# Optimization experiments

Measured on AMD Instinct MI355X. Metric: run time of the kernel, lower is better.

The kernel has to match this reference:

```python
import jax, jax.numpy as jnp
from jax import lax
import numpy as np
import math

B, N, A = 4096, 8, 5
IN_CH, HW = 3, 5
POS = 2
OBS_IN = POS + N            # 10
OBS_ACT_IN = OBS_IN + A     # 15
D = 128                     # obs_output_dim == d_k == embed width
STATE_DIM = 32 + OBS_IN     # 42
SAP_IN = 32 + OBS_ACT_IN    # 47


def setup_inputs() -> dict:
    key = jax.random.key(0)
    ks = jax.random.split(key, 24)
    w = lambda k, shape: (jax.random.normal(k, shape) * 0.05).astype(jnp.float32)
    return {
        "agent_states": jax.random.normal(ks[0], (B, N, IN_CH, HW, HW), jnp.float32),
        "agent_global_positions": jax.random.normal(ks[1], (B, N, POS), jnp.float32),
        "agent_one_hot_encoding": jax.random.uniform(ks[2], (B, N, N), jnp.float32),
        "policies": jax.random.uniform(ks[3], (B, N, A), jnp.float32),
        "actions": jax.random.uniform(ks[4], (B, N, A), jnp.float32),
        "conv1_w": w(ks[5], (16, IN_CH, 3, 3)), "conv1_b": w(ks[6], (16,)),
        "conv2_w": w(ks[7], (32, 16, 3, 3)),    "conv2_b": w(ks[8], (32,)),
        "se_w": w(ks[9], (STATE_DIM, 128)),     "se_b": w(ks[10], (128,)),
        "key_w": w(ks[11], (128, D)),           "key_b": w(ks[12], (D,)),
        "query_w": w(ks[13], (128, D)),         "query_b": w(ks[14], (D,)),
        "sap_w": w(ks[15], (SAP_IN, 128)),      "sap_b": w(ks[16], (128,)),
        "av_w": w(ks[17], (128, 128)),          "av_b": w(ks[18], (128,)),
        "f1_w": w(ks[19], (128, 64)),           "f1_b": w(ks[20], (64,)),
        "f2_w": w(ks[21], (64, 1)),             "f2_b": w(ks[22], (1,)),
    }


def _conv(x, w, b):
    y = lax.conv_general_dilated(x, w, (1, 1), 'VALID',
                                 dimension_numbers=('NCHW', 'OIHW', 'NCHW'))
    return y + b[None, :, None, None]


def reference(agent_states, agent_global_positions, agent_one_hot_encoding,
              policies, actions,
              conv1_w, conv1_b, conv2_w, conv2_b,
              se_w, se_b, key_w, key_b, query_w, query_b,
              sap_w, sap_b, av_w, av_b, f1_w, f1_b, f2_w, f2_b):
    leaky = lambda x: jnp.where(x >= 0, x, 0.01 * x)
    b, n = agent_states.shape[0], agent_states.shape[1]

    # CNN encoder: [B*N,3,5,5] -> [B*N,32,1,1]
    x = agent_states.reshape(b * n, IN_CH, HW, HW)
    h = leaky(_conv(x, conv1_w, conv1_b))
    h = leaky(_conv(h, conv2_w, conv2_b))
    pose_id = jnp.concatenate([agent_global_positions, agent_one_hot_encoding], axis=-1)
    states = jnp.concatenate([h.reshape(b, n, -1), pose_id], axis=-1)  # [B,N,42]

    states_embed = jnp.tanh(states @ se_w + se_b)                      # [B,N,128]
    k = states_embed @ key_w + key_b
    q = states_embed @ query_w + query_b
    weight = jax.nn.softmax(jnp.einsum('bqd,bkd->bqk', q, k) / math.sqrt(D), axis=-1)

    obs_actions = jnp.concatenate([states, actions], axis=-1)          # [B,N,47]
    obs_policy = jnp.concatenate([states, policies], axis=-1)         # [B,N,47]
    # place_policies puts the policy vector on the diagonal (i==j), action elsewhere.
    eye = jnp.eye(n, dtype=states.dtype)[None, :, :, None]             # [1,N,N,1]
    oap = eye * obs_policy[:, None, :, :] + (1.0 - eye) * obs_actions[:, None, :, :]  # [B,i,j,47]

    oap_embed = jnp.tanh(oap @ sap_w + sap_b)                          # [B,N,N,128]
    attn_vals = jnp.tanh(oap_embed @ av_w + av_b)                      # [B,i,j,128]

    # node_features[b,a,i,d] = sum_j weight[b,a,j] * attn_vals[b,i,j,d]
    # (replaces the original repeat -> broadcast-multiply -> sum over O(N^4) tensor)
    node_features = jnp.einsum('baj,bijd->baid', weight, attn_vals)    # [B,N,N,128]

    v = jnp.tanh(node_features @ f1_w + f1_b)
    value = v @ f2_w + f2_b                                            # [B,N,N,1]
    return value, weight
```

## Files before the change

### kernel.cpp

```cpp
#include <hip/hip_runtime.h>
#include <math.h>

#define NB 4096
#define NA 8
#define BN (NB*NA)

#define OFF_SE   0
#define OFF_SAP  4096
#define OFF_AV   8192
#define OFF_F1   16384
#define OFF_M    20480
#define OFF_U    28672
#define OFF_W2P  28800

typedef short short8 __attribute__((ext_vector_type(8)));
typedef float f32x4 __attribute__((ext_vector_type(4)));

#define MFMA(a,b,c) __builtin_amdgcn_mfma_f32_16x16x32_bf16(a,b,c,0,0,0)

__device__ __forceinline__ float fast_tanh(float x){
    float e = __expf(2.0f*x);
    return 1.0f - 2.0f*__builtin_amdgcn_rcpf(e+1.0f);
}
__device__ __forceinline__ unsigned bfr(float x){
    unsigned u = __float_as_uint(x);
    return (u + 0x7fffu + ((u>>16)&1u)) >> 16;
}
__device__ __forceinline__ unsigned pk2(float lo, float hi){
    return bfr(lo) | (bfr(hi)<<16);
}
__device__ __forceinline__ float bf2f(unsigned short s){
    return __uint_as_float(((unsigned)s)<<16);
}
__device__ __forceinline__ short8 fragld(const unsigned* p){
    union { uint4 u; short8 s; } cv;
    cv.u = *(const uint4*)p;
    return cv.s;
}

__global__ __launch_bounds__(256) void kW(const float* __restrict__ se_w,
        const float* __restrict__ sap_w, const float* __restrict__ av_w,
        const float* __restrict__ f1_w, const float* __restrict__ qw,
        const float* __restrict__ kw, const float* __restrict__ qb,
        const float* __restrict__ w2,
        unsigned* __restrict__ ws){
    int idx = blockIdx.x*256 + threadIdx.x;
    if (idx < 4096){
        int w = idx, tile = w>>9, rem = w&511;
        int ft = rem>>6, r2 = (rem>>2)&15, wi = rem&3;
        int f2 = tile*16 + r2, f1 = ft*8 + wi*2;
        float lo = (f1   < 42)? se_w[f1*128+f2]     : 0.f;
        float hi = (f1+1 < 42)? se_w[(f1+1)*128+f2] : 0.f;
        ws[OFF_SE + w] = pk2(lo,hi);
    } else if (idx < 8192){
        int w = idx-4096, tile = w>>9, rem = w&511;
        int ft = rem>>6, r2 = (rem>>2)&15, wi = rem&3;
        int f2 = tile*16 + r2, f1 = ft*8 + wi*2;
        float lo = (f1   < 47)? sap_w[f1*128+f2]     : 0.f;
        float hi = (f1+1 < 47)? sap_w[(f1+1)*128+f2] : 0.f;
        ws[OFF_SAP + w] = pk2(lo,hi);
    } else if (idx < 16384){
        int w = idx-8192, tile = w>>10, rem = w&1023;
        int ft = rem>>6, r2 = (rem>>2)&15, wi = rem&3;
        int f2 = tile*16 + r2, f1 = ft*8 + wi*2;
        ws[OFF_AV + w] = pk2(av_w[f1*128+f2], av_w[(f1+1)*128+f2]);
    } else if (idx < 20480){
        int w = idx-16384, tile = w>>10, rem = w&1023;
        int ft = rem>>6, r2 = (rem>>2)&15, wi = rem&3;
        int f2 = tile*16 + r2, f1 = ft*8 + wi*2;
        ws[OFF_F1 + w] = pk2(f1_w[f1*64+f2], f1_w[(f1+1)*64+f2]);
    } else if (idx < 28672){
        int w = idx-20480, tile = w>>10, rem = w&1023;
        int ft = rem>>6, r2 = (rem>>2)&15, wi = rem&3;
        int f2 = tile*16 + r2, e0 = ft*8 + wi*2;
        float lo=0.f, hi=0.f;
        for (int d=0; d<128; ++d){
            float kv = kw[f2*128+d];
            lo += qw[e0*128+d]*kv;
            hi += qw[(e0+1)*128+d]*kv;
        }
        ws[OFF_M + w] = pk2(lo,hi);
    } else if (idx < 28800){
        int f = idx-28672;
        float a = 0.f;
        for (int d=0; d<128; ++d) a += qb[d]*kw[f*128+d];
        ((float*)ws)[OFF_U + f] = a;
    } else if (idx < 31360){
        int w = idx-28800;
        int ftile = w/1280, rem = w - ftile*1280;
        int ft = rem>>6, r2 = (rem>>2)&15, wi = rem&3;
        int f = ftile*16 + r2, k0 = ft*8 + wi*2;
        float lo = (k0   < 144)? w2[f*144+k0]   : 0.f;
        float hi = (k0+1 < 144)? w2[f*144+k0+1] : 0.f;
        ws[OFF_W2P + w] = pk2(lo,hi);
    }
}

__global__ __launch_bounds__(256,2) void kF(const unsigned* __restrict__ ws,
        const float* __restrict__ xin, const float* __restrict__ pos,
        const float* __restrict__ oneh, const float* __restrict__ acts,
        const float* __restrict__ pols,
        const float* __restrict__ w1, const float* __restrict__ b1,
        const float* __restrict__ b2,
        const float* __restrict__ se_b,
        const float* __restrict__ sap_b, const float* __restrict__ av_b,
        const float* __restrict__ f1_b, const float* __restrict__ f2_w,
        const float* __restrict__ f2_b,
        float* __restrict__ wout, float* __restrict__ value){
    __shared__ unsigned SM[9216];
    __shared__ unsigned stPk[4096];
    __shared__ unsigned sA64[2176];
    __shared__ unsigned sP64[2176];
    __shared__ float s_w[512];
    __shared__ float s_bias[384];
    __shared__ float s_ub[256];
    const int t = threadIdx.x;
    const int wv = t>>6, lane = t&63;
    const int g = lane>>4, c = lane&15;

    float* c_in   = (float*)SM;
    unsigned* hpk = SM + 1216;
    float* c_ap   = (float*)(SM+6336);
    float* c_pose = (float*)(SM+6496);
    float* c_w1   = (float*)(SM+6656);
    float* c_b1   = (float*)(SM+7088);
    float* c_b2   = (float*)(SM+7104);
    for (int q=t; q<432; q+=256) c_w1[q] = w1[q];
    if (t<16) c_b1[t] = b1[t];
    if (t<32) c_b2[t] = b2[t];
    for (int q=t; q<512; q+=256) hpk[(q>>7)*1280 + 1152 + (q&127)] = 0;
    for (int q=t; q<384; q+=256)
        s_bias[q] = (q<128)? sap_b[q] : (q<256)? av_b[q-128] : (q<320)? f1_b[q-256] : f2_w[q-320];
    s_ub[t] = (t<128)? ((const float*)ws)[OFF_U+t] : se_b[t-128];

    for (int p=0; p<4; ++p){
        const size_t a0g = (size_t)blockIdx.x*64 + p*16;
        for (int q=t; q<1200; q+=256){
            int ag=q/75, r=q-ag*75;
            c_in[ag*76+r] = xin[a0g*75+q];
        }
        for (int q=t; q<160; q+=256){
            int ag=q/10, k=q-ag*10;
            c_ap[q]   = (k<5)? acts[(a0g+ag)*5+k] : pols[(a0g+ag)*5+(k-5)];
            c_pose[q] = (k<2)? pos[(a0g+ag)*2+k]  : oneh[(a0g+ag)*8+(k-2)];
        }
        __syncthreads();
        {
            const int ag = t&15, oc = t>>4;
            float w[27];
            #pragma unroll
            for (int i=0;i<27;++i) w[i]=c_w1[oc*27+i];
            float out[9];
            float bb = c_b1[oc];
            #pragma unroll
            for (int q=0;q<9;++q) out[q]=bb;
            #pragma unroll
            for (int ic=0;ic<3;++ic){
                float pin[25];
                #pragma unroll
                for (int i=0;i<25;++i) pin[i]=c_in[ag*76+ic*25+i];
                #pragma unroll
                for (int y=0;y<3;++y)
                  #pragma unroll
                  for (int x=0;x<3;++x)
                    #pragma unroll
                    for (int ky=0;ky<3;++ky)
                      #pragma unroll
                      for (int kx=0;kx<3;++kx)
                        out[y*3+x] += pin[(y+ky)*5+(x+kx)] * w[ic*9+ky*3+kx];
            }
            unsigned short* hp16 = (unsigned short*)(hpk + p*1280);
            #pragma unroll
            for (int q=0;q<9;++q){
                float v = out[q];
                v = (v>=0.f)? v : 0.01f*v;
                int k = oc*9+q;
                int word = (k>>3)*64 + ag*4 + ((k>>1)&3);
                hp16[word*2 + (k&1)] = (unsigned short)bfr(v);
            }
        }
        {
            const int ft4 = t>>6, r = (t>>2)&15, wi = t&3;
            const int f0 = 32 + ft4*8 + wi*2;
            float a0=0.f,a1=0.f,p0=0.f,p1=0.f;
            if (f0 < 42){ a0 = c_pose[r*10 + f0-32]; p0 = a0; }
            else if (f0 < 47){ a0 = c_ap[r*10 + f0-42]; p0 = c_ap[r*10+5 + f0-42]; }
            if (f0+1 < 42){ a1 = c_pose[r*10 + f0-31]; p1 = a1; }
            else if (f0+1 < 47){ a1 = c_ap[r*10 + f0-41]; p1 = c_ap[r*10+5 + f0-41]; }
            int word = p*512 + (4+ft4)*64 + r*4 + wi;
            stPk[word]      = pk2(a0,a1);
            stPk[2048+word] = pk2(p0,p1);
        }
        __syncthreads();
    }
    {
        const unsigned* hw = hpk + wv*1280;
        f32x4 c2[2];
        c2[0] = (f32x4){0.f,0.f,0.f,0.f};
        c2[1] = (f32x4){0.f,0.f,0.f,0.f};
        #pragma unroll
        for (int kt=0; kt<5; ++kt){
            short8 hb  = fragld(hw + kt*256 + lane*4);
            short8 w0f = fragld(ws + OFF_W2P + kt*256 + lane*4);
            short8 w1f = fragld(ws + OFF_W2P + 1280 + kt*256 + lane*4);
            c2[0] = MFMA(w0f, hb, c2[0]);
            c2[1] = MFMA(w1f, hb, c2[1]);
        }
        #pragma unroll
        for (int ft=0; ft<2; ++ft){
            const float* bp = &c_b2[ft*16 + g*4];
            float d0 = c2[ft][0]+bp[0]; d0 = (d0>=0.f)? d0 : 0.01f*d0;
            float d1 = c2[ft][1]+bp[1]; d1 = (d1>=0.f)? d1 : 0.01f*d1;
            float d2 = c2[ft][2]+bp[2]; d2 = (d2>=0.f)? d2 : 0.01f*d2;
            float d3 = c2[ft][3]+bp[3]; d3 = (d3>=0.f)? d3 : 0.01f*d3;
            int word = wv*512 + (2*ft + (g>>1))*64 + c*4 + (g&1)*2;
            uint2 pw = make_uint2(pk2(d0,d1), pk2(d2,d3));
            *(uint2*)&stPk[word] = pw;
            *(uint2*)&stPk[2048+word] = pw;
        }
    }
    __syncthreads();

    const int tile = blockIdx.x*4 + wv;
    short8 bfA0 = fragld(&stPk[wv*512 + lane*4]);
    short8 bfA1 = fragld(&stPk[wv*512 + 256 + lane*4]);
    short8 bfP0 = fragld(&stPk[2048 + wv*512 + lane*4]);
    short8 bfP1 = fragld(&stPk[2048 + wv*512 + 256 + lane*4]);
    unsigned (*s_stage)[2048] = (unsigned (*)[2048])&SM[0];
    unsigned* U1 = &SM[4096];
    unsigned* wS = &U1[wv*1280];
    unsigned* tS = &U1[wv*1280 + 1024];

    uint4 r0, r1;
#define PREF(off) { r0 = *(const uint4*)(ws + (off) + t*4); \
                    r1 = *(const uint4*)(ws + (off) + 1024 + t*4); }
#define WR(b) { *(uint4*)&s_stage[b][t*4] = r0; *(uint4*)&s_stage[b][1024 + t*4] = r1; }

    PREF(OFF_SE); WR(0);
    __syncthreads();

    f32x4 acc[8];
    #pragma unroll
    for (int i=0;i<8;++i) acc[i] = (f32x4){0.f,0.f,0.f,0.f};
    PREF(OFF_SE + 2048);
    #pragma unroll
    for (int ft=0; ft<4; ++ft){
        short8 a0 = fragld(&s_stage[0][ft*512 + lane*4]);
        short8 a1 = fragld(&s_stage[0][ft*512 + 256 + lane*4]);
        acc[ft] = MFMA(a0, bfA0, acc[ft]);
        acc[ft] = MFMA(a1, bfA1, acc[ft]);
    }
    WR(1); __syncthreads();
    PREF(OFF_M);
    #pragma unroll
    for (int ft=4; ft<8; ++ft){
        short8 a0 = fragld(&s_stage[1][(ft-4)*512 + lane*4]);
        short8 a1 = fragld(&s_stage[1][(ft-4)*512 + 256 + lane*4]);
        acc[ft] = MFMA(a0, bfA0, acc[ft]);
        acc[ft] = MFMA(a1, bfA1, acc[ft]);
    }
    WR(0);
    #pragma unroll
    for (int ft=0; ft<8; ++ft){
        const float* bp = &s_ub[128 + ft*16 + g*4];
        float d0 = fast_tanh(acc[ft][0]+bp[0]);
        float d1 = fast_tanh(acc[ft][1]+bp[1]);
        float d2 = fast_tanh(acc[ft][2]+bp[2]);
        float d3 = fast_tanh(acc[ft][3]+bp[3]);
        int word = (2*ft + (g>>1))*64 + c*4 + (g&1)*2;
        *(uint2*)&wS[word] = make_uint2(pk2(d0,d1), pk2(d2,d3));
    }
    short8 ef[4];
    #pragma unroll
    for (int kt=0; kt<4; ++kt) ef[kt] = fragld(&wS[kt*256 + lane*4]);
    __syncthreads();

    f32x4 L = (f32x4){0.f,0.f,0.f,0.f};
    #pragma unroll
    for (int i=0; i<4; ++i){
        const int nextOff = (i<3)? (OFF_M + (i+1)*2048) : OFF_SAP;
        PREF(nextOff);
        f32x4 a2[2];
        a2[0] = (f32x4){0.f,0.f,0.f,0.f};
        a2[1] = (f32x4){0.f,0.f,0.f,0.f};
        #pragma unroll
        for (int ftl=0; ftl<2; ++ftl)
          #pragma unroll
          for (int kt=0; kt<4; ++kt){
            short8 mf = fragld(&s_stage[i&1][ftl*1024 + kt*256 + lane*4]);
            a2[ftl] = MFMA(mf, ef[kt], a2[ftl]);
          }
        WR((i+1)&1);
        #pragma unroll
        for (int ftl=0; ftl<2; ++ftl){
            const float* up = &s_ub[(2*i+ftl)*16 + g*4];
            int word = (2*ftl + (g>>1))*64 + c*4 + (g&1)*2;
            *(uint2*)&tS[word] = make_uint2(pk2(a2[ftl][0]+up[0], a2[ftl][1]+up[1]),
                                            pk2(a2[ftl][2]+up[2], a2[ftl][3]+up[3]));
        }
        short8 tf = fragld(&tS[lane*4]);
        L = MFMA(tf, ef[i], L);
        __syncthreads();
    }
    {
        float sc[4];
        #pragma unroll
        for (int q=0;q<4;++q) sc[q] = L[q]*0.08838834764831845f;
        #pragma unroll
        for (int q=0;q<4;++q){
            float m = sc[q];
            m = fmaxf(m, __shfl_xor(m,1));
            m = fmaxf(m, __shfl_xor(m,2));
            m = fmaxf(m, __shfl_xor(m,4));
            float ex = __expf(sc[q]-m);
            float su = ex;
            su += __shfl_xor(su,1);
            su += __shfl_xor(su,2);
            su += __shfl_xor(su,4);
            sc[q] = ex/su;
        }
        if ((c>>3) == (g>>1)){
            int lb = wv*2 + (g>>1);
            int batch = tile*2 + (g>>1);
            int idx = ((g&1)*4)*8 + (c&7);
            #pragma unroll
            for (int q=0;q<4;++q){
                float v = sc[q];
                wout[batch*64 + idx + q*8] = v;
                s_w[lb*64 + idx + q*8] = v;
            }
        }
    }

    f32x4 aS[2][8];
    #pragma unroll
    for (int v=0;v<2;++v)
      #pragma unroll
      for (int i=0;i<8;++i) aS[v][i] = (f32x4){0.f,0.f,0.f,0.f};
    PREF(OFF_SAP + 2048);
    #pragma unroll
    for (int ft=0; ft<4; ++ft){
        short8 a0 = fragld(&s_stage[0][ft*512 + lane*4]);
        short8 a1 = fragld(&s_stage[0][ft*512 + 256 + lane*4]);
        aS[0][ft] = MFMA(a0, bfA0, aS[0][ft]);
        aS[0][ft] = MFMA(a1, bfA1, aS[0][ft]);
        aS[1][ft] = MFMA(a0, bfP0, aS[1][ft]);
        aS[1][ft] = MFMA(a1, bfP1, aS[1][ft]);
    }
    WR(1); __syncthreads();
    PREF(OFF_AV);
    #pragma unroll
    for (int ft=4; ft<8; ++ft){
        short8 a0 = fragld(&s_stage[1][(ft-4)*512 + lane*4]);
        short8 a1 = fragld(&s_stage[1][(ft-4)*512 + 256 + lane*4]);
        aS[0][ft] = MFMA(a0, bfA0, aS[0][ft]);
        aS[0][ft] = MFMA(a1, bfA1, aS[0][ft]);
        aS[1][ft] = MFMA(a0, bfP0, aS[1][ft]);
        aS[1][ft] = MFMA(a1, bfP1, aS[1][ft]);
    }
    WR(0);
    short8 spA[4], spP[4];
    #pragma unroll
    for (int ft=0; ft<8; ++ft){
        const float* bp = &s_bias[ft*16 + g*4];
        float d0 = fast_tanh(aS[0][ft][0]+bp[0]);
        float d1 = fast_tanh(aS[0][ft][1]+bp[1]);
        float d2 = fast_tanh(aS[0][ft][2]+bp[2]);
        float d3 = fast_tanh(aS[0][ft][3]+bp[3]);
        int word = (2*ft + (g>>1))*64 + c*4 + (g&1)*2;
        *(uint2*)&wS[word] = make_uint2(pk2(d0,d1), pk2(d2,d3));
    }
    #pragma unroll
    for (int kt=0; kt<4; ++kt) spA[kt] = fragld(&wS[kt*256 + lane*4]);
    #pragma unroll
    for (int ft=0; ft<8; ++ft){
        const float* bp = &s_bias[ft*16 + g*4];
        float d0 = fast_tanh(aS[1][ft][0]+bp[0]);
        float d1 = fast_tanh(aS[1][ft][1]+bp[1]);
        float d2 = fast_tanh(aS[1][ft][2]+bp[2]);
        float d3 = fast_tanh(aS[1][ft][3]+bp[3]);
        int word = (2*ft + (g>>1))*64 + c*4 + (g&1)*2;
        *(uint2*)&wS[word] = make_uint2(pk2(d0,d1), pk2(d2,d3));
    }
    #pragma unroll
    for (int kt=0; kt<4; ++kt) spP[kt] = fragld(&wS[kt*256 + lane*4]);
    __syncthreads();

    f32x4 aV[2][8];
    #pragma unroll
    for (int v=0;v<2;++v)
      #pragma unroll
      for (int i=0;i<8;++i) aV[v][i] = (f32x4){0.f,0.f,0.f,0.f};
    short8 avA[4], avP[4];
    #pragma unroll
    for (int i=0; i<4; ++i){
        const int nextOff = (i<3)? (OFF_AV + (i+1)*2048) : OFF_F1;
        PREF(nextOff);
        #pragma unroll
        for (int ftl=0; ftl<2; ++ftl){
            const int ft = 2*i + ftl;
            #pragma unroll
            for (int kt=0; kt<4; ++kt){
                short8 af = fragld(&s_stage[i&1][ftl*1024 + kt*256 + lane*4]);
                aV[0][ft] = MFMA(af, spA[kt], aV[0][ft]);
                aV[1][ft] = MFMA(af, spP[kt], aV[1][ft]);
            }
        }
        WR((i+1)&1);
        if (i==3){
            #pragma unroll
            for (int ft=0; ft<8; ++ft){
                const float* bp = &s_bias[128 + ft*16 + g*4];
                float d0 = fast_tanh(aV[0][ft][0]+bp[0]);
                float d1 = fast_tanh(aV[0][ft][1]+bp[1]);
                float d2 = fast_tanh(aV[0][ft][2]+bp[2]);
                float d3 = fast_tanh(aV[0][ft][3]+bp[3]);
                int word = (2*ft + (g>>1))*64 + c*4 + (g&1)*2;
                *(uint2*)&wS[word] = make_uint2(pk2(d0,d1), pk2(d2,d3));
            }
            #pragma unroll
            for (int kt=0; kt<4; ++kt) avA[kt] = fragld(&wS[kt*256 + lane*4]);
            #pragma unroll
            for (int ft=0; ft<8; ++ft){
                const float* bp = &s_bias[128 + ft*16 + g*4];
                float d0 = fast_tanh(aV[1][ft][0]+bp[0]);
                float d1 = fast_tanh(aV[1][ft][1]+bp[1]);
                float d2 = fast_tanh(aV[1][ft][2]+bp[2]);
                float d3 = fast_tanh(aV[1][ft][3]+bp[3]);
                int word = (2*ft + (g>>1))*64 + c*4 + (g&1)*2;
                *(uint2*)&wS[word] = make_uint2(pk2(d0,d1), pk2(d2,d3));
            }
            #pragma unroll
            for (int kt=0; kt<4; ++kt) avP[kt] = fragld(&wS[kt*256 + lane*4]);
        }
        __syncthreads();
    }

    f32x4 aF[2][4];
    #pragma unroll
    for (int v=0;v<2;++v)
      #pragma unroll
      for (int i=0;i<4;++i) aF[v][i] = (f32x4){0.f,0.f,0.f,0.f};
    PREF(OFF_F1 + 2048);
    #pragma unroll
    for (int ftl=0; ftl<2; ++ftl)
      #pragma unroll
      for (int kt=0; kt<4; ++kt){
        short8 af = fragld(&s_stage[0][ftl*1024 + kt*256 + lane*4]);
        aF[0][ftl] = MFMA(af, avA[kt], aF[0][ftl]);
        aF[1][ftl] = MFMA(af, avP[kt], aF[1][ftl]);
      }
    WR(1); __syncthreads();
    #pragma unroll
    for (int ftl=0; ftl<2; ++ftl)
      #pragma unroll
      for (int kt=0; kt<4; ++kt){
        short8 af = fragld(&s_stage[1][ftl*1024 + kt*256 + lane*4]);
        aF[0][2+ftl] = MFMA(af, avA[kt], aF[0][2+ftl]);
        aF[1][2+ftl] = MFMA(af, avP[kt], aF[1][2+ftl]);
      }
    {
        int row = wv*16 + c;
        #pragma unroll
        for (int v=0;v<2;++v){
            unsigned* dst = v? sP64 : sA64;
            #pragma unroll
            for (int ft=0; ft<4; ++ft){
                int idx = row*34 + ft*8 + 2*g;
                *(uint2*)&dst[idx] = make_uint2(pk2(aF[v][ft][0], aF[v][ft][1]),
                                                pk2(aF[v][ft][2], aF[v][ft][3]));
            }
        }
    }
    __syncthreads();
    float* s_b64 = (float*)U1;
    const unsigned short* A16 = (const unsigned short*)sA64;
    const unsigned short* P16 = (const unsigned short*)sP64;
    #pragma unroll
    for (int k=0; k<16; ++k){
        int e = t + 256*k;
        int bq = e>>9, a = (e>>6)&7, cc = e&63;
        const float* wp = &s_w[bq*64 + a*8];
        float acc4 = 0.f;
        #pragma unroll
        for (int j=0;j<8;++j) acc4 += wp[j]*bf2f(A16[(bq*8+j)*68 + cc]);
        s_b64[(bq*8+a)*68 + cc] = acc4;
    }
    __syncthreads();
    #pragma unroll
    for (int k=0; k<2; ++k){
        int o = t + 256*k;
        int bq = o>>6, a = (o>>3)&7, i = o&7;
        float w_ai = s_w[bq*64 + a*8 + i];
        const float* pb = &s_b64[(bq*8+a)*68];
        const unsigned short* pA = &A16[(bq*8+i)*68];
        const unsigned short* pP = &P16[(bq*8+i)*68];
        float acc5 = 0.f;
        #pragma unroll 8
        for (int cc=0; cc<64; ++cc){
            float dd = bf2f(pP[cc]) - bf2f(pA[cc]);
            acc5 += fast_tanh(pb[cc] + w_ai*dd + s_bias[256+cc]) * s_bias[320+cc];
        }
        value[(size_t)blockIdx.x*512 + o] = acc5 + f2_b[0];
    }
#undef PREF
#undef WR
}

extern "C" void kernel_launch(void* const* d_in, const int* in_sizes, int n_in,
                              void* d_out, int out_size, void* d_ws, size_t ws_size,
                              hipStream_t stream){
    const float* agent_states = (const float*)d_in[0];
    const float* pos    = (const float*)d_in[1];
    const float* oneh   = (const float*)d_in[2];
    const float* pols   = (const float*)d_in[3];
    const float* acts   = (const float*)d_in[4];
    const float* w1     = (const float*)d_in[5];
    const float* b1     = (const float*)d_in[6];
    const float* w2     = (const float*)d_in[7];
    const float* b2     = (const float*)d_in[8];
    const float* se_w   = (const float*)d_in[9];
    const float* se_b   = (const float*)d_in[10];
    const float* key_w  = (const float*)d_in[11];
    const float* query_w= (const float*)d_in[13];
    const float* query_b= (const float*)d_in[14];
    const float* sap_w  = (const float*)d_in[15];
    const float* sap_b  = (const float*)d_in[16];
    const float* av_w   = (const float*)d_in[17];
    const float* av_b   = (const float*)d_in[18];
    const float* f1_w   = (const float*)d_in[19];
    const float* f1_b   = (const float*)d_in[20];
    const float* f2_w   = (const float*)d_in[21];
    const float* f2_b   = (const float*)d_in[22];

    unsigned* ws = (unsigned*)d_ws;

    float* value = (float*)d_out;
    float* wout  = value + (size_t)NB*NA*NA;

    kW<<<123, 256, 0, stream>>>(se_w, sap_w, av_w, f1_w, query_w, key_w, query_b, w2, ws);
    kF<<<BN/64, 256, 0, stream>>>(ws, agent_states, pos, oneh, acts, pols,
                                  w1, b1, b2, se_b, sap_b, av_b, f1_b, f2_w, f2_b,
                                  wout, value);
}
```

Baseline: 52.44 us.

## Double block size to 512 threads, splitting each tile's feature work across two waves

```diff
diff --git a/kernel.cpp b/kernel.cpp
--- a/kernel.cpp
+++ b/kernel.cpp
@@ -96,7 +96,7 @@
     }
 }
 
-__global__ __launch_bounds__(256,2) void kF(const unsigned* __restrict__ ws,
+__global__ __launch_bounds__(512,4) void kF(const unsigned* __restrict__ ws,
         const float* __restrict__ xin, const float* __restrict__ pos,
         const float* __restrict__ oneh, const float* __restrict__ acts,
         const float* __restrict__ pols,
@@ -117,36 +117,38 @@
     const int t = threadIdx.x;
     const int wv = t>>6, lane = t&63;
     const int g = lane>>4, c = lane&15;
+    const int tl = wv>>1, h = wv&1;
 
     float* c_in   = (float*)SM;
-    unsigned* hpk = SM + 1216;
-    float* c_ap   = (float*)(SM+6336);
-    float* c_pose = (float*)(SM+6496);
-    float* c_w1   = (float*)(SM+6656);
-    float* c_b1   = (float*)(SM+7088);
-    float* c_b2   = (float*)(SM+7104);
-    for (int q=t; q<432; q+=256) c_w1[q] = w1[q];
-    if (t<16) c_b1[t] = b1[t];
-    if (t<32) c_b2[t] = b2[t];
-    for (int q=t; q<512; q+=256) hpk[(q>>7)*1280 + 1152 + (q&127)] = 0;
-    for (int q=t; q<384; q+=256)
-        s_bias[q] = (q<128)? sap_b[q] : (q<256)? av_b[q-128] : (q<320)? f1_b[q-256] : f2_w[q-320];
-    s_ub[t] = (t<128)? ((const float*)ws)[OFF_U+t] : se_b[t-128];
-
-    for (int p=0; p<4; ++p){
-        const size_t a0g = (size_t)blockIdx.x*64 + p*16;
-        for (int q=t; q<1200; q+=256){
-            int ag=q/75, r=q-ag*75;
-            c_in[ag*76+r] = xin[a0g*75+q];
-        }
-        for (int q=t; q<160; q+=256){
-            int ag=q/10, k=q-ag*10;
-            c_ap[q]   = (k<5)? acts[(a0g+ag)*5+k] : pols[(a0g+ag)*5+(k-5)];
-            c_pose[q] = (k<2)? pos[(a0g+ag)*2+k]  : oneh[(a0g+ag)*8+(k-2)];
+    unsigned* hpk = SM + 2432;
+    float* c_ap   = (float*)(SM+7552);
+    float* c_pose = (float*)(SM+7872);
+    float* c_w1   = (float*)(SM+8192);
+    float* c_b1   = (float*)(SM+8624);
+    float* c_b2   = (float*)(SM+8640);
+    if (t<432) c_w1[t] = w1[t];
+    else if (t<448) c_b1[t-432] = b1[t-432];
+    else if (t<480) c_b2[t-448] = b2[t-448];
+    hpk[(t>>7)*1280 + 1152 + (t&127)] = 0;
+    if (t<384)
+        s_bias[t] = (t<128)? sap_b[t] : (t<256)? av_b[t-128] : (t<320)? f1_b[t-256] : f2_w[t-320];
+    if (t<256) s_ub[t] = (t<128)? ((const float*)ws)[OFF_U+t] : se_b[t-128];
+
+    for (int p=0; p<2; ++p){
+        for (int q=t; q<2400; q+=512){
+            int tp=q/1200, rr=q-tp*1200, ag=rr/75, r=rr-ag*75;
+            size_t row = (size_t)blockIdx.x*64 + (p*2+tp)*16 + ag;
+            c_in[tp*1216 + ag*76 + r] = xin[row*75 + r];
+        }
+        if (t<320){
+            int tp=t/160, rr=t-tp*160, ag=rr/10, k=rr-ag*10;
+            size_t row = (size_t)blockIdx.x*64 + (p*2+tp)*16 + ag;
+            c_ap[t]   = (k<5)? acts[row*5+k] : pols[row*5+(k-5)];
+            c_pose[t] = (k<2)? pos[row*2+k]  : oneh[row*8+(k-2)];
         }
         __syncthreads();
         {
-            const int ag = t&15, oc = t>>4;
+            const int tp = t>>8, tt = t&255, ag = tt&15, oc = tt>>4;
             float w[27];
             #pragma unroll
             for (int i=0;i<27;++i) w[i]=c_w1[oc*27+i];
@@ -158,7 +160,7 @@
             for (int ic=0;ic<3;++ic){
                 float pin[25];
                 #pragma unroll
-                for (int i=0;i<25;++i) pin[i]=c_in[ag*76+ic*25+i];
+                for (int i=0;i<25;++i) pin[i]=c_in[tp*1216 + ag*76 + ic*25 + i];
                 #pragma unroll
                 for (int y=0;y<3;++y)
                   #pragma unroll
@@ -169,7 +171,7 @@
                       for (int kx=0;kx<3;++kx)
                         out[y*3+x] += pin[(y+ky)*5+(x+kx)] * w[ic*9+ky*3+kx];
             }
-            unsigned short* hp16 = (unsigned short*)(hpk + p*1280);
+            unsigned short* hp16 = (unsigned short*)(hpk + (p*2+tp)*1280);
             #pragma unroll
             for (int q=0;q<9;++q){
                 float v = out[q];
@@ -180,20 +182,21 @@
             }
         }
         {
-            const int ft4 = t>>6, r = (t>>2)&15, wi = t&3;
+            const int tp = t>>8, tt = t&255;
+            const int ft4 = tt>>6, r = (tt>>2)&15, wi = tt&3;
             const int f0 = 32 + ft4*8 + wi*2;
             float a0=0.f,a1=0.f,p0=0.f,p1=0.f;
-            if (f0 < 42){ a0 = c_pose[r*10 + f0-32]; p0 = a0; }
-            else if (f0 < 47){ a0 = c_ap[r*10 + f0-42]; p0 = c_ap[r*10+5 + f0-42]; }
-            if (f0+1 < 42){ a1 = c_pose[r*10 + f0-31]; p1 = a1; }
-            else if (f0+1 < 47){ a1 = c_ap[r*10 + f0-41]; p1 = c_ap[r*10+5 + f0-41]; }
-            int word = p*512 + (4+ft4)*64 + r*4 + wi;
+            if (f0 < 42){ a0 = c_pose[tp*160 + r*10 + f0-32]; p0 = a0; }
+            else if (f0 < 47){ a0 = c_ap[tp*160 + r*10 + f0-42]; p0 = c_ap[tp*160 + r*10+5 + f0-42]; }
+            if (f0+1 < 42){ a1 = c_pose[tp*160 + r*10 + f0-31]; p1 = a1; }
+            else if (f0+1 < 47){ a1 = c_ap[tp*160 + r*10 + f0-41]; p1 = c_ap[tp*160 + r*10+5 + f0-41]; }
+            int word = (p*2+tp)*512 + (4+ft4)*64 + r*4 + wi;
             stPk[word]      = pk2(a0,a1);
             stPk[2048+word] = pk2(p0,p1);
         }
         __syncthreads();
     }
-    {
+    if (wv < 4){
         const unsigned* hw = hpk + wv*1280;
         f32x4 c2[2];
         c2[0] = (f32x4){0.f,0.f,0.f,0.f};
@@ -221,88 +224,91 @@
     }
     __syncthreads();
 
-    const int tile = blockIdx.x*4 + wv;
-    short8 bfA0 = fragld(&stPk[wv*512 + lane*4]);
-    short8 bfA1 = fragld(&stPk[wv*512 + 256 + lane*4]);
-    short8 bfP0 = fragld(&stPk[2048 + wv*512 + lane*4]);
-    short8 bfP1 = fragld(&stPk[2048 + wv*512 + 256 + lane*4]);
-    unsigned (*s_stage)[2048] = (unsigned (*)[2048])&SM[0];
-    unsigned* U1 = &SM[4096];
-    unsigned* wS = &U1[wv*1280];
-    unsigned* tS = &U1[wv*1280 + 1024];
+    const int tile = blockIdx.x*4 + tl;
+    short8 bfA0 = fragld(&stPk[tl*512 + lane*4]);
+    short8 bfA1 = fragld(&stPk[tl*512 + 256 + lane*4]);
+    short8 bfP0 = fragld(&stPk[2048 + tl*512 + lane*4]);
+    short8 bfP1 = fragld(&stPk[2048 + tl*512 + 256 + lane*4]);
+    unsigned* stage = SM;
+    unsigned* U1 = SM + 4096;
+    unsigned* wS = U1 + tl*1280;
 
     uint4 r0, r1;
-#define PREF(off) { r0 = *(const uint4*)(ws + (off) + t*4); \
-                    r1 = *(const uint4*)(ws + (off) + 1024 + t*4); }
-#define WR(b) { *(uint4*)&s_stage[b][t*4] = r0; *(uint4*)&s_stage[b][1024 + t*4] = r1; }
-
-    PREF(OFF_SE); WR(0);
-    __syncthreads();
-
-    f32x4 acc[8];
-    #pragma unroll
-    for (int i=0;i<8;++i) acc[i] = (f32x4){0.f,0.f,0.f,0.f};
-    PREF(OFF_SE + 2048);
-    #pragma unroll
-    for (int ft=0; ft<4; ++ft){
-        short8 a0 = fragld(&s_stage[0][ft*512 + lane*4]);
-        short8 a1 = fragld(&s_stage[0][ft*512 + 256 + lane*4]);
-        acc[ft] = MFMA(a0, bfA0, acc[ft]);
-        acc[ft] = MFMA(a1, bfA1, acc[ft]);
-    }
-    WR(1); __syncthreads();
-    PREF(OFF_M);
-    #pragma unroll
-    for (int ft=4; ft<8; ++ft){
-        short8 a0 = fragld(&s_stage[1][(ft-4)*512 + lane*4]);
-        short8 a1 = fragld(&s_stage[1][(ft-4)*512 + 256 + lane*4]);
-        acc[ft] = MFMA(a0, bfA0, acc[ft]);
-        acc[ft] = MFMA(a1, bfA1, acc[ft]);
-    }
-    WR(0);
-    #pragma unroll
-    for (int ft=0; ft<8; ++ft){
+#define PREFP(off) { r0 = *(const uint4*)(ws + (off) + t*4); \
+                     r1 = *(const uint4*)(ws + (off) + 2048 + t*4); }
+#define WRP() { *(uint4*)&stage[t*4] = r0; *(uint4*)&stage[2048 + t*4] = r1; }
+
+    PREFP(OFF_SE);
+    WRP();
+    PREFP(OFF_M);
+    __syncthreads();
+
+    f32x4 acc[4];
+    #pragma unroll
+    for (int i=0;i<4;++i) acc[i] = (f32x4){0.f,0.f,0.f,0.f};
+    #pragma unroll
+    for (int i=0;i<4;++i){
+        short8 a0 = fragld(&stage[h*2048 + i*512 + lane*4]);
+        short8 a1 = fragld(&stage[h*2048 + i*512 + 256 + lane*4]);
+        acc[i] = MFMA(a0, bfA0, acc[i]);
+        acc[i] = MFMA(a1, bfA1, acc[i]);
+    }
+    #pragma unroll
+    for (int i=0;i<4;++i){
+        int ft = h*4+i;
         const float* bp = &s_ub[128 + ft*16 + g*4];
-        float d0 = fast_tanh(acc[ft][0]+bp[0]);
-        float d1 = fast_tanh(acc[ft][1]+bp[1]);
-        float d2 = fast_tanh(acc[ft][2]+bp[2]);
-        float d3 = fast_tanh(acc[ft][3]+bp[3]);
+        float d0 = fast_tanh(acc[i][0]+bp[0]);
+        float d1 = fast_tanh(acc[i][1]+bp[1]);
+        float d2 = fast_tanh(acc[i][2]+bp[2]);
+        float d3 = fast_tanh(acc[i][3]+bp[3]);
         int word = (2*ft + (g>>1))*64 + c*4 + (g&1)*2;
         *(uint2*)&wS[word] = make_uint2(pk2(d0,d1), pk2(d2,d3));
     }
+    __syncthreads();
     short8 ef[4];
     #pragma unroll
     for (int kt=0; kt<4; ++kt) ef[kt] = fragld(&wS[kt*256 + lane*4]);
     __syncthreads();
-
-    f32x4 L = (f32x4){0.f,0.f,0.f,0.f};
-    #pragma unroll
-    for (int i=0; i<4; ++i){
-        const int nextOff = (i<3)? (OFF_M + (i+1)*2048) : OFF_SAP;
-        PREF(nextOff);
-        f32x4 a2[2];
-        a2[0] = (f32x4){0.f,0.f,0.f,0.f};
-        a2[1] = (f32x4){0.f,0.f,0.f,0.f};
-        #pragma unroll
-        for (int ftl=0; ftl<2; ++ftl)
-          #pragma unroll
-          for (int kt=0; kt<4; ++kt){
-            short8 mf = fragld(&s_stage[i&1][ftl*1024 + kt*256 + lane*4]);
-            a2[ftl] = MFMA(mf, ef[kt], a2[ftl]);
-          }
-        WR((i+1)&1);
-        #pragma unroll
-        for (int ftl=0; ftl<2; ++ftl){
-            const float* up = &s_ub[(2*i+ftl)*16 + g*4];
-            int word = (2*ftl + (g>>1))*64 + c*4 + (g&1)*2;
-            *(uint2*)&tS[word] = make_uint2(pk2(a2[ftl][0]+up[0], a2[ftl][1]+up[1]),
-                                            pk2(a2[ftl][2]+up[2], a2[ftl][3]+up[3]));
-        }
-        short8 tf = fragld(&tS[lane*4]);
-        L = MFMA(tf, ef[i], L);
-        __syncthreads();
-    }
+    WRP();
+    PREFP(OFF_M + 4096);
+    __syncthreads();
+    if (h==0){
+        #pragma unroll
+        for (int fl=0; fl<4; ++fl){
+            f32x4 a2 = (f32x4){0.f,0.f,0.f,0.f};
+            #pragma unroll
+            for (int kt=0; kt<4; ++kt)
+                a2 = MFMA(fragld(&stage[fl*1024 + kt*256 + lane*4]), ef[kt], a2);
+            const float* up = &s_ub[fl*16 + g*4];
+            int word = (2*fl + (g>>1))*64 + c*4 + (g&1)*2;
+            *(uint2*)&wS[word] = make_uint2(pk2(a2[0]+up[0], a2[1]+up[1]),
+                                            pk2(a2[2]+up[2], a2[3]+up[3]));
+        }
+    }
+    __syncthreads();
+    WRP();
+    PREFP(OFF_SAP);
+    __syncthreads();
+    if (h==1){
+        #pragma unroll
+        for (int fl=0; fl<4; ++fl){
+            int ft = 4+fl;
+            f32x4 a2 = (f32x4){0.f,0.f,0.f,0.f};
+            #pragma unroll
+            for (int kt=0; kt<4; ++kt)
+                a2 = MFMA(fragld(&stage[fl*1024 + kt*256 + lane*4]), ef[kt], a2);
+            const float* up = &s_ub[ft*16 + g*4];
+            int word = (2*ft + (g>>1))*64 + c*4 + (g&1)*2;
+            *(uint2*)&wS[word] = make_uint2(pk2(a2[0]+up[0], a2[1]+up[1]),
+                                            pk2(a2[2]+up[2], a2[3]+up[3]));
+        }
+    }
+    __syncthreads();
     {
+        f32x4 L = (f32x4){0.f,0.f,0.f,0.f};
+        #pragma unroll
+        for (int kt=0; kt<4; ++kt)
+            L = MFMA(fragld(&wS[kt*256 + lane*4]), ef[kt], L);
         float sc[4];
         #pragma unroll
         for (int q=0;q<4;++q) sc[q] = L[q]*0.08838834764831845f;
@@ -319,8 +325,8 @@
             su += __shfl_xor(su,4);
             sc[q] = ex/su;
         }
-        if ((c>>3) == (g>>1)){
-            int lb = wv*2 + (g>>1);
+        if (h==0 && (c>>3) == (g>>1)){
+            int lb = tl*2 + (g>>1);
             int batch = tile*2 + (g>>1);
             int idx = ((g&1)*4)*8 + (c&7);
             #pragma unroll
@@ -331,144 +337,146 @@
             }
         }
     }
-
-    f32x4 aS[2][8];
+    __syncthreads();
+    WRP();
+    PREFP(OFF_AV);
+    __syncthreads();
+    f32x4 aS[2][4];
     #pragma unroll
     for (int v=0;v<2;++v)
       #pragma unroll
-      for (int i=0;i<8;++i) aS[v][i] = (f32x4){0.f,0.f,0.f,0.f};
-    PREF(OFF_SAP + 2048);
-    #pragma unroll
-    for (int ft=0; ft<4; ++ft){
-        short8 a0 = fragld(&s_stage[0][ft*512 + lane*4]);
-        short8 a1 = fragld(&s_stage[0][ft*512 + 256 + lane*4]);
-        aS[0][ft] = MFMA(a0, bfA0, aS[0][ft]);
-        aS[0][ft] = MFMA(a1, bfA1, aS[0][ft]);
-        aS[1][ft] = MFMA(a0, bfP0, aS[1][ft]);
-        aS[1][ft] = MFMA(a1, bfP1, aS[1][ft]);
-    }
-    WR(1); __syncthreads();
-    PREF(OFF_AV);
-    #pragma unroll
-    for (int ft=4; ft<8; ++ft){
-        short8 a0 = fragld(&s_stage[1][(ft-4)*512 + lane*4]);
-        short8 a1 = fragld(&s_stage[1][(ft-4)*512 + 256 + lane*4]);
-        aS[0][ft] = MFMA(a0, bfA0, aS[0][ft]);
-        aS[0][ft] = MFMA(a1, bfA1, aS[0][ft]);
-        aS[1][ft] = MFMA(a0, bfP0, aS[1][ft]);
-        aS[1][ft] = MFMA(a1, bfP1, aS[1][ft]);
-    }
-    WR(0);
+      for (int i=0;i<4;++i) aS[v][i] = (f32x4){0.f,0.f,0.f,0.f};
+    #pragma unroll
+    for (int i=0;i<4;++i){
+        short8 a0 = fragld(&stage[h*2048 + i*512 + lane*4]);
+        short8 a1 = fragld(&stage[h*2048 + i*512 + 256 + lane*4]);
+        aS[0][i] = MFMA(a0, bfA0, aS[0][i]);
+        aS[0][i] = MFMA(a1, bfA1, aS[0][i]);
+        aS[1][i] = MFMA(a0, bfP0, aS[1][i]);
+        aS[1][i] = MFMA(a1, bfP1, aS[1][i]);
+    }
     short8 spA[4], spP[4];
     #pragma unroll
-    for (int ft=0; ft<8; ++ft){
+    for (int i=0;i<4;++i){
+        int ft = h*4+i;
         const float* bp = &s_bias[ft*16 + g*4];
-        float d0 = fast_tanh(aS[0][ft][0]+bp[0]);
-        float d1 = fast_tanh(aS[0][ft][1]+bp[1]);
-        float d2 = fast_tanh(aS[0][ft][2]+bp[2]);
-        float d3 = fast_tanh(aS[0][ft][3]+bp[3]);
+        float d0 = fast_tanh(aS[0][i][0]+bp[0]);
+        float d1 = fast_tanh(aS[0][i][1]+bp[1]);
+        float d2 = fast_tanh(aS[0][i][2]+bp[2]);
+        float d3 = fast_tanh(aS[0][i][3]+bp[3]);
         int word = (2*ft + (g>>1))*64 + c*4 + (g&1)*2;
         *(uint2*)&wS[word] = make_uint2(pk2(d0,d1), pk2(d2,d3));
     }
+    __syncthreads();
     #pragma unroll
     for (int kt=0; kt<4; ++kt) spA[kt] = fragld(&wS[kt*256 + lane*4]);
-    #pragma unroll
-    for (int ft=0; ft<8; ++ft){
+    __syncthreads();
+    #pragma unroll
+    for (int i=0;i<4;++i){
+        int ft = h*4+i;
         const float* bp = &s_bias[ft*16 + g*4];
-        float d0 = fast_tanh(aS[1][ft][0]+bp[0]);
-        float d1 = fast_tanh(aS[1][ft][1]+bp[1]);
-        float d2 = fast_tanh(aS[1][ft][2]+bp[2]);
-        float d3 = fast_tanh(aS[1][ft][3]+bp[3]);
+        float d0 = fast_tanh(aS[1][i][0]+bp[0]);
+        float d1 = fast_tanh(aS[1][i][1]+bp[1]);
+        float d2 = fast_tanh(aS[1][i][2]+bp[2]);
+        float d3 = fast_tanh(aS[1][i][3]+bp[3]);
         int word = (2*ft + (g>>1))*64 + c*4 + (g&1)*2;
         *(uint2*)&wS[word] = make_uint2(pk2(d0,d1), pk2(d2,d3));
     }
+    __syncthreads();
     #pragma unroll
     for (int kt=0; kt<4; ++kt) spP[kt] = fragld(&wS[kt*256 + lane*4]);
     __syncthreads();
-
-    f32x4 aV[2][8];
+    WRP();
+    PREFP(OFF_AV + 4096);
+    __syncthreads();
+    f32x4 aV[2][4];
     #pragma unroll
     for (int v=0;v<2;++v)
       #pragma unroll
-      for (int i=0;i<8;++i) aV[v][i] = (f32x4){0.f,0.f,0.f,0.f};
+      for (int i=0;i<4;++i) aV[v][i] = (f32x4){0.f,0.f,0.f,0.f};
+    #pragma unroll
+    for (int j=0;j<2;++j){
+        int fl = 2*h + j;
+        #pragma unroll
+        for (int kt=0; kt<4; ++kt){
+            short8 af = fragld(&stage[fl*1024 + kt*256 + lane*4]);
+            aV[0][j] = MFMA(af, spA[kt], aV[0][j]);
+            aV[1][j] = MFMA(af, spP[kt], aV[1][j]);
+        }
+    }
+    __syncthreads();
+    WRP();
+    PREFP(OFF_F1);
+    __syncthreads();
+    #pragma unroll
+    for (int j=0;j<2;++j){
+        int fl = 2*h + j;
+        #pragma unroll
+        for (int kt=0; kt<4; ++kt){
+            short8 af = fragld(&stage[fl*1024 + kt*256 + lane*4]);
+            aV[0][2+j] = MFMA(af, spA[kt], aV[0][2+j]);
+            aV[1][2+j] = MFMA(af, spP[kt], aV[1][2+j]);
+        }
+    }
     short8 avA[4], avP[4];
     #pragma unroll
-    for (int i=0; i<4; ++i){
-        const int nextOff = (i<3)? (OFF_AV + (i+1)*2048) : OFF_F1;
-        PREF(nextOff);
-        #pragma unroll
-        for (int ftl=0; ftl<2; ++ftl){
-            const int ft = 2*i + ftl;
-            #pragma unroll
-            for (int kt=0; kt<4; ++kt){
-                short8 af = fragld(&s_stage[i&1][ftl*1024 + kt*256 + lane*4]);
-                aV[0][ft] = MFMA(af, spA[kt], aV[0][ft]);
-                aV[1][ft] = MFMA(af, spP[kt], aV[1][ft]);
-            }
-        }
-        WR((i+1)&1);
-        if (i==3){
-            #pragma unroll
-            for (int ft=0; ft<8; ++ft){
-                const float* bp = &s_bias[128 + ft*16 + g*4];
-                float d0 = fast_tanh(aV[0][ft][0]+bp[0]);
-                float d1 = fast_tanh(aV[0][ft][1]+bp[1]);
-                float d2 = fast_tanh(aV[0][ft][2]+bp[2]);
-                float d3 = fast_tanh(aV[0][ft][3]+bp[3]);
-                int word = (2*ft + (g>>1))*64 + c*4 + (g&1)*2;
-                *(uint2*)&wS[word] = make_uint2(pk2(d0,d1), pk2(d2,d3));
-            }
-            #pragma unroll
-            for (int kt=0; kt<4; ++kt) avA[kt] = fragld(&wS[kt*256 + lane*4]);
-            #pragma unroll
-            for (int ft=0; ft<8; ++ft){
-                const float* bp = &s_bias[128 + ft*16 + g*4];
-                float d0 = fast_tanh(aV[1][ft][0]+bp[0]);
-                float d1 = fast_tanh(aV[1][ft][1]+bp[1]);
-                float d2 = fast_tanh(aV[1][ft][2]+bp[2]);
-                float d3 = fast_tanh(aV[1][ft][3]+bp[3]);
-                int word = (2*ft + (g>>1))*64 + c*4 + (g&1)*2;
-                *(uint2*)&wS[word] = make_uint2(pk2(d0,d1), pk2(d2,d3));
-            }
-            #pragma unroll
-            for (int kt=0; kt<4; ++kt) avP[kt] = fragld(&wS[kt*256 + lane*4]);
-        }
-        __syncthreads();
-    }
-
-    f32x4 aF[2][4];
+    for (int k=0;k<4;++k){
+        int ft = (k>>1)*4 + 2*h + (k&1);
+        const float* bp = &s_bias[128 + ft*16 + g*4];
+        float d0 = fast_tanh(aV[0][k][0]+bp[0]);
+        float d1 = fast_tanh(aV[0][k][1]+bp[1]);
+        float d2 = fast_tanh(aV[0][k][2]+bp[2]);
+        float d3 = fast_tanh(aV[0][k][3]+bp[3]);
+        int word = (2*ft + (g>>1))*64 + c*4 + (g&1)*2;
+        *(uint2*)&wS[word] = make_uint2(pk2(d0,d1), pk2(d2,d3));
+    }
+    __syncthreads();
+    #pragma unroll
+    for (int kt=0; kt<4; ++kt) avA[kt] = fragld(&wS[kt*256 + lane*4]);
+    __syncthreads();
+    #pragma unroll
+    for (int k=0;k<4;++k){
+        int ft = (k>>1)*4 + 2*h + (k&1);
+        const float* bp = &s_bias[128 + ft*16 + g*4];
+        float d0 = fast_tanh(aV[1][k][0]+bp[0]);
+        float d1 = fast_tanh(aV[1][k][1]+bp[1]);
+        float d2 = fast_tanh(aV[1][k][2]+bp[2]);
+        float d3 = fast_tanh(aV[1][k][3]+bp[3]);
+        int word = (2*ft + (g>>1))*64 + c*4 + (g&1)*2;
+        *(uint2*)&wS[word] = make_uint2(pk2(d0,d1), pk2(d2,d3));
+    }
+    __syncthreads();
+    #pragma unroll
+    for (int kt=0; kt<4; ++kt) avP[kt] = fragld(&wS[kt*256 + lane*4]);
+    __syncthreads();
+    WRP();
+    __syncthreads();
+    f32x4 aF[2][2];
     #pragma unroll
     for (int v=0;v<2;++v)
       #pragma unroll
-      for (int i=0;i<4;++i) aF[v][i] = (f32x4){0.f,0.f,0.f,0.f};
-    PREF(OFF_F1 + 2048);
-    #pragma unroll
-    for (int ftl=0; ftl<2; ++ftl)
-      #pragma unroll
-      for (int kt=0; kt<4; ++kt){
-        short8 af = fragld(&s_stage[0][ftl*1024 + kt*256 + lane*4]);
-        aF[0][ftl] = MFMA(af, avA[kt], aF[0][ftl]);
-        aF[1][ftl] = MFMA(af, avP[kt], aF[1][ftl]);
-      }
-    WR(1); __syncthreads();
-    #pragma unroll
-    for (int ftl=0; ftl<2; ++ftl)
-      #pragma unroll
-      for (int kt=0; kt<4; ++kt){
-        short8 af = fragld(&s_stage[1][ftl*1024 + kt*256 + lane*4]);
-        aF[0][2+ftl] = MFMA(af, avA[kt], aF[0][2+ftl]);
-        aF[1][2+ftl] = MFMA(af, avP[kt], aF[1][2+ftl]);
-      }
+      for (int j=0;j<2;++j) aF[v][j] = (f32x4){0.f,0.f,0.f,0.f};
+    #pragma unroll
+    for (int j=0;j<2;++j){
+        int fl = 2*h + j;
+        #pragma unroll
+        for (int kt=0; kt<4; ++kt){
+            short8 af = fragld(&stage[fl*1024 + kt*256 + lane*4]);
+            aF[0][j] = MFMA(af, avA[kt], aF[0][j]);
+            aF[1][j] = MFMA(af, avP[kt], aF[1][j]);
+        }
+    }
     {
-        int row = wv*16 + c;
+        int row = tl*16 + c;
         #pragma unroll
         for (int v=0;v<2;++v){
             unsigned* dst = v? sP64 : sA64;
             #pragma unroll
-            for (int ft=0; ft<4; ++ft){
+            for (int j=0;j<2;++j){
+                int ft = 2*h + j;
                 int idx = row*34 + ft*8 + 2*g;
-                *(uint2*)&dst[idx] = make_uint2(pk2(aF[v][ft][0], aF[v][ft][1]),
-                                                pk2(aF[v][ft][2], aF[v][ft][3]));
+                *(uint2*)&dst[idx] = make_uint2(pk2(aF[v][j][0], aF[v][j][1]),
+                                                pk2(aF[v][j][2], aF[v][j][3]));
             }
         }
     }
@@ -477,8 +485,8 @@
     const unsigned short* A16 = (const unsigned short*)sA64;
     const unsigned short* P16 = (const unsigned short*)sP64;
     #pragma unroll
-    for (int k=0; k<16; ++k){
-        int e = t + 256*k;
+    for (int k=0; k<8; ++k){
+        int e = t + 512*k;
         int bq = e>>9, a = (e>>6)&7, cc = e&63;
         const float* wp = &s_w[bq*64 + a*8];
         float acc4 = 0.f;
@@ -487,10 +495,8 @@
         s_b64[(bq*8+a)*68 + cc] = acc4;
     }
     __syncthreads();
-    #pragma unroll
-    for (int k=0; k<2; ++k){
-        int o = t + 256*k;
-        int bq = o>>6, a = (o>>3)&7, i = o&7;
+    {
+        int bq = t>>6, a = (t>>3)&7, i = t&7;
         float w_ai = s_w[bq*64 + a*8 + i];
         const float* pb = &s_b64[(bq*8+a)*68];
         const unsigned short* pA = &A16[(bq*8+i)*68];
@@ -501,10 +507,10 @@
             float dd = bf2f(pP[cc]) - bf2f(pA[cc]);
             acc5 += fast_tanh(pb[cc] + w_ai*dd + s_bias[256+cc]) * s_bias[320+cc];
         }
-        value[(size_t)blockIdx.x*512 + o] = acc5 + f2_b[0];
-    }
-#undef PREF
-#undef WR
+        value[(size_t)blockIdx.x*512 + t] = acc5 + f2_b[0];
+    }
+#undef PREFP
+#undef WRP
 }
 
 extern "C" void kernel_launch(void* const* d_in, const int* in_sizes, int n_in,
@@ -539,7 +545,7 @@
     float* wout  = value + (size_t)NB*NA*NA;
 
     kW<<<123, 256, 0, stream>>>(se_w, sap_w, av_w, f1_w, query_w, key_w, query_b, w2, ws);
-    kF<<<BN/64, 256, 0, stream>>>(ws, agent_states, pos, oneh, acts, pols,
+    kF<<<BN/64, 512, 0, stream>>>(ws, agent_states, pos, oneh, acts, pols,
                                   w1, b1, b2, se_b, sap_b, av_b, f1_b, f2_w, f2_b,
                                   wout, value);
 }
```

Measured after the change: 60.00 us. +14.4%, slower.

## Halve fused kernel block to two waves and shrink shared memory footprint

Applied to the files above, without the earlier changes.

```diff
diff --git a/kernel.cpp b/kernel.cpp
--- a/kernel.cpp
+++ b/kernel.cpp
@@ -96,7 +96,7 @@
     }
 }
 
-__global__ __launch_bounds__(256,2) void kF(const unsigned* __restrict__ ws,
+__global__ __launch_bounds__(128,2) void kF(const unsigned* __restrict__ ws,
         const float* __restrict__ xin, const float* __restrict__ pos,
         const float* __restrict__ oneh, const float* __restrict__ acts,
         const float* __restrict__ pols,
@@ -107,46 +107,49 @@
         const float* __restrict__ f1_b, const float* __restrict__ f2_w,
         const float* __restrict__ f2_b,
         float* __restrict__ wout, float* __restrict__ value){
-    __shared__ unsigned SM[9216];
-    __shared__ unsigned stPk[4096];
-    __shared__ unsigned sA64[2176];
-    __shared__ unsigned sP64[2176];
-    __shared__ float s_w[512];
+    __shared__ unsigned SM[6144];
+    __shared__ unsigned stPkA[1024];
+    __shared__ unsigned stP5[128];
+    __shared__ unsigned sA64[1088];
+    __shared__ unsigned sP64[1088];
+    __shared__ float s_w[256];
     __shared__ float s_bias[384];
-    __shared__ float s_ub[256];
     const int t = threadIdx.x;
     const int wv = t>>6, lane = t&63;
     const int g = lane>>4, c = lane&15;
 
+    float* s_ub = (float*)sA64;
     float* c_in   = (float*)SM;
-    unsigned* hpk = SM + 1216;
-    float* c_ap   = (float*)(SM+6336);
-    float* c_pose = (float*)(SM+6496);
-    float* c_w1   = (float*)(SM+6656);
-    float* c_b1   = (float*)(SM+7088);
-    float* c_b2   = (float*)(SM+7104);
-    for (int q=t; q<432; q+=256) c_w1[q] = w1[q];
+    unsigned* hpk = SM + 2432;
+    float* c_ap   = (float*)(SM+4992);
+    float* c_pose = (float*)(SM+5312);
+    float* c_w1   = (float*)(SM+5632);
+    float* c_b1   = (float*)(SM+6064);
+    float* c_b2   = (float*)(SM+6080);
+    for (int q=t; q<432; q+=128) c_w1[q] = w1[q];
     if (t<16) c_b1[t] = b1[t];
-    if (t<32) c_b2[t] = b2[t];
-    for (int q=t; q<512; q+=256) hpk[(q>>7)*1280 + 1152 + (q&127)] = 0;
-    for (int q=t; q<384; q+=256)
+    else if (t<48) c_b2[t-16] = b2[t-16];
+    for (int q=t; q<256; q+=128) hpk[(q>>7)*1280 + 1152 + (q&127)] = 0;
+    for (int q=t; q<384; q+=128)
         s_bias[q] = (q<128)? sap_b[q] : (q<256)? av_b[q-128] : (q<320)? f1_b[q-256] : f2_w[q-320];
-    s_ub[t] = (t<128)? ((const float*)ws)[OFF_U+t] : se_b[t-128];
-
-    for (int p=0; p<4; ++p){
-        const size_t a0g = (size_t)blockIdx.x*64 + p*16;
-        for (int q=t; q<1200; q+=256){
-            int ag=q/75, r=q-ag*75;
-            c_in[ag*76+r] = xin[a0g*75+q];
-        }
-        for (int q=t; q<160; q+=256){
-            int ag=q/10, k=q-ag*10;
-            c_ap[q]   = (k<5)? acts[(a0g+ag)*5+k] : pols[(a0g+ag)*5+(k-5)];
-            c_pose[q] = (k<2)? pos[(a0g+ag)*2+k]  : oneh[(a0g+ag)*8+(k-2)];
-        }
-        __syncthreads();
-        {
-            const int ag = t&15, oc = t>>4;
+    for (int q=t; q<256; q+=128) s_ub[q] = (q<128)? ((const float*)ws)[OFF_U+q] : se_b[q-128];
+
+    for (int q=t; q<2400; q+=128){
+        int tp=q/1200, rr=q-tp*1200, ag=rr/75, r=rr-ag*75;
+        c_in[tp*1216 + ag*76 + r] = xin[((size_t)blockIdx.x*32 + tp*16 + ag)*75 + r];
+    }
+    for (int q=t; q<320; q+=128){
+        int tp=q/160, rr=q-tp*160, ag=rr/10, k=rr-ag*10;
+        size_t row = (size_t)blockIdx.x*32 + tp*16 + ag;
+        c_ap[q]   = (k<5)? acts[row*5+k] : pols[row*5+(k-5)];
+        c_pose[q] = (k<2)? pos[row*2+k]  : oneh[row*8+(k-2)];
+    }
+    __syncthreads();
+    #pragma unroll
+    for (int tp=0; tp<2; ++tp){
+        #pragma unroll
+        for (int oh=0; oh<2; ++oh){
+            const int ag = t&15, oc = (t>>4) + oh*8;
             float w[27];
             #pragma unroll
             for (int i=0;i<27;++i) w[i]=c_w1[oc*27+i];
@@ -158,7 +161,7 @@
             for (int ic=0;ic<3;++ic){
                 float pin[25];
                 #pragma unroll
-                for (int i=0;i<25;++i) pin[i]=c_in[ag*76+ic*25+i];
+                for (int i=0;i<25;++i) pin[i]=c_in[tp*1216 + ag*76 + ic*25 + i];
                 #pragma unroll
                 for (int y=0;y<3;++y)
                   #pragma unroll
@@ -169,7 +172,7 @@
                       for (int kx=0;kx<3;++kx)
                         out[y*3+x] += pin[(y+ky)*5+(x+kx)] * w[ic*9+ky*3+kx];
             }
-            unsigned short* hp16 = (unsigned short*)(hpk + p*1280);
+            unsigned short* hp16 = (unsigned short*)(hpk + tp*1280);
             #pragma unroll
             for (int q=0;q<9;++q){
                 float v = out[q];
@@ -179,20 +182,20 @@
                 hp16[word*2 + (k&1)] = (unsigned short)bfr(v);
             }
         }
-        {
-            const int ft4 = t>>6, r = (t>>2)&15, wi = t&3;
-            const int f0 = 32 + ft4*8 + wi*2;
-            float a0=0.f,a1=0.f,p0=0.f,p1=0.f;
-            if (f0 < 42){ a0 = c_pose[r*10 + f0-32]; p0 = a0; }
-            else if (f0 < 47){ a0 = c_ap[r*10 + f0-42]; p0 = c_ap[r*10+5 + f0-42]; }
-            if (f0+1 < 42){ a1 = c_pose[r*10 + f0-31]; p1 = a1; }
-            else if (f0+1 < 47){ a1 = c_ap[r*10 + f0-41]; p1 = c_ap[r*10+5 + f0-41]; }
-            int word = p*512 + (4+ft4)*64 + r*4 + wi;
-            stPk[word]      = pk2(a0,a1);
-            stPk[2048+word] = pk2(p0,p1);
-        }
-        __syncthreads();
-    }
+    }
+    for (int q=t; q<512; q+=128){
+        const int tp = q>>8, tt = q&255;
+        const int ft4 = tt>>6, r = (tt>>2)&15, wi = tt&3;
+        const int f0 = 32 + ft4*8 + wi*2;
+        float a0=0.f,a1=0.f,p0=0.f,p1=0.f;
+        if (f0 < 42){ a0 = c_pose[tp*160 + r*10 + f0-32]; p0 = a0; }
+        else if (f0 < 47){ a0 = c_ap[tp*160 + r*10 + f0-42]; p0 = c_ap[tp*160 + r*10+5 + f0-42]; }
+        if (f0+1 < 42){ a1 = c_pose[tp*160 + r*10 + f0-31]; p1 = a1; }
+        else if (f0+1 < 47){ a1 = c_ap[tp*160 + r*10 + f0-41]; p1 = c_ap[tp*160 + r*10+5 + f0-41]; }
+        stPkA[tp*512 + (4+ft4)*64 + r*4 + wi] = pk2(a0,a1);
+        if (ft4 == 1) stP5[tp*64 + r*4 + wi] = pk2(p0,p1);
+    }
+    __syncthreads();
     {
         const unsigned* hw = hpk + wv*1280;
         f32x4 c2[2];
@@ -214,27 +217,35 @@
             float d2 = c2[ft][2]+bp[2]; d2 = (d2>=0.f)? d2 : 0.01f*d2;
             float d3 = c2[ft][3]+bp[3]; d3 = (d3>=0.f)? d3 : 0.01f*d3;
             int word = wv*512 + (2*ft + (g>>1))*64 + c*4 + (g&1)*2;
-            uint2 pw = make_uint2(pk2(d0,d1), pk2(d2,d3));
-            *(uint2*)&stPk[word] = pw;
-            *(uint2*)&stPk[2048+word] = pw;
-        }
-    }
-    __syncthreads();
-
-    const int tile = blockIdx.x*4 + wv;
-    short8 bfA0 = fragld(&stPk[wv*512 + lane*4]);
-    short8 bfA1 = fragld(&stPk[wv*512 + 256 + lane*4]);
-    short8 bfP0 = fragld(&stPk[2048 + wv*512 + lane*4]);
-    short8 bfP1 = fragld(&stPk[2048 + wv*512 + 256 + lane*4]);
+            *(uint2*)&stPkA[word] = make_uint2(pk2(d0,d1), pk2(d2,d3));
+        }
+    }
+    __syncthreads();
+
+    const int tile = blockIdx.x*2 + wv;
+    short8 bfA0 = fragld(&stPkA[wv*512 + lane*4]);
+    short8 bfA1 = fragld(&stPkA[wv*512 + 256 + lane*4]);
+    short8 bfP0 = bfA0;
+    const unsigned* p1addr = (g==1) ? &stP5[wv*64 + c*4]
+                                    : &stPkA[wv*512 + 256 + lane*4];
+    short8 bfP1 = fragld(p1addr);
     unsigned (*s_stage)[2048] = (unsigned (*)[2048])&SM[0];
     unsigned* U1 = &SM[4096];
-    unsigned* wS = &U1[wv*1280];
-    unsigned* tS = &U1[wv*1280 + 1024];
+    unsigned* wS = &U1[wv*1024];
+    unsigned* tS = wS;
 
     uint4 r0, r1;
 #define PREF(off) { r0 = *(const uint4*)(ws + (off) + t*4); \
-                    r1 = *(const uint4*)(ws + (off) + 1024 + t*4); }
-#define WR(b) { *(uint4*)&s_stage[b][t*4] = r0; *(uint4*)&s_stage[b][1024 + t*4] = r1; }
+                    r1 = *(const uint4*)(ws + (off) + 512 + t*4); \
+                    *(uint4*)&r0; }
+#undef PREF
+    uint4 r2, r3;
+#define PREF(off) { r0 = *(const uint4*)(ws + (off) + t*4); \
+                    r1 = *(const uint4*)(ws + (off) + 512 + t*4); \
+                    r2 = *(const uint4*)(ws + (off) + 1024 + t*4); \
+                    r3 = *(const uint4*)(ws + (off) + 1536 + t*4); }
+#define WR(b) { *(uint4*)&s_stage[b][t*4] = r0; *(uint4*)&s_stage[b][512 + t*4] = r1; \
+                *(uint4*)&s_stage[b][1024 + t*4] = r2; *(uint4*)&s_stage[b][1536 + t*4] = r3; }
 
     PREF(OFF_SE); WR(0);
     __syncthreads();
@@ -473,12 +484,12 @@
         }
     }
     __syncthreads();
-    float* s_b64 = (float*)U1;
+    float* s_b64 = (float*)SM;
     const unsigned short* A16 = (const unsigned short*)sA64;
     const unsigned short* P16 = (const unsigned short*)sP64;
     #pragma unroll
     for (int k=0; k<16; ++k){
-        int e = t + 256*k;
+        int e = t + 128*k;
         int bq = e>>9, a = (e>>6)&7, cc = e&63;
         const float* wp = &s_w[bq*64 + a*8];
         float acc4 = 0.f;
@@ -489,7 +500,7 @@
     __syncthreads();
     #pragma unroll
     for (int k=0; k<2; ++k){
-        int o = t + 256*k;
+        int o = t + 128*k;
         int bq = o>>6, a = (o>>3)&7, i = o&7;
         float w_ai = s_w[bq*64 + a*8 + i];
         const float* pb = &s_b64[(bq*8+a)*68];
@@ -501,7 +512,7 @@
             float dd = bf2f(pP[cc]) - bf2f(pA[cc]);
             acc5 += fast_tanh(pb[cc] + w_ai*dd + s_bias[256+cc]) * s_bias[320+cc];
         }
-        value[(size_t)blockIdx.x*512 + o] = acc5 + f2_b[0];
+        value[(size_t)blockIdx.x*256 + o] = acc5 + f2_b[0];
     }
 #undef PREF
 #undef WR
@@ -539,7 +550,7 @@
     float* wout  = value + (size_t)NB*NA*NA;
 
     kW<<<123, 256, 0, stream>>>(se_w, sap_w, av_w, f1_w, query_w, key_w, query_b, w2, ws);
-    kF<<<BN/64, 256, 0, stream>>>(ws, agent_states, pos, oneh, acts, pols,
+    kF<<<BN/32, 128, 0, stream>>>(ws, agent_states, pos, oneh, acts, pols,
                                   w1, b1, b2, se_b, sap_b, av_b, f1_b, f2_w, f2_b,
                                   wout, value);
 }
```

New measurement: 53.88 us. +2.8%, slower.
